# Kernel optimization log

Hardware: AMD Instinct MI355X
Metric: run time of the kernel (lower is better)

Reference implementation:

```python
import jax, jax.numpy as jnp
import numpy as np
from functools import partial

P = 14          # patch size
IMG = 448       # image size
D = 1152        # hidden dim
H = 16          # num heads
DH = D // H     # head dim = 72
I = 4304        # intermediate dim
L = 4           # num layers
N = (IMG // P) ** 2  # 1024 patches
EPS = 1e-6


def setup_inputs() -> dict:
    key = jax.random.key(0)
    ks = jax.random.split(key, 24)
    s = 0.02
    inp = {
        "images": jax.random.normal(ks[0], (2, 2, IMG, IMG, 3), jnp.float32),
        "conv_w": jax.random.normal(ks[1], (P, P, 3, D), jnp.float32) * s,
        "conv_b": jnp.zeros((D,), jnp.float32),
        "pos_emb": jax.random.normal(ks[2], (N, D), jnp.float32) * s,
        # per-layer stacked parameters, leading axis L
        "ln1_g": jnp.ones((L, D), jnp.float32),
        "ln1_b": jnp.zeros((L, D), jnp.float32),
        "Wq": jax.random.normal(ks[3], (L, D, D), jnp.float32) * s,
        "bq": jnp.zeros((L, D), jnp.float32),
        "Wk": jax.random.normal(ks[4], (L, D, D), jnp.float32) * s,
        "bk": jnp.zeros((L, D), jnp.float32),
        "Wv": jax.random.normal(ks[5], (L, D, D), jnp.float32) * s,
        "bv": jnp.zeros((L, D), jnp.float32),
        "Wo": jax.random.normal(ks[6], (L, D, D), jnp.float32) * s,
        "bo": jnp.zeros((L, D), jnp.float32),
        "ln2_g": jnp.ones((L, D), jnp.float32),
        "ln2_b": jnp.zeros((L, D), jnp.float32),
        "W1": jax.random.normal(ks[7], (L, D, I), jnp.float32) * s,
        "b1": jnp.zeros((L, I), jnp.float32),
        "W2": jax.random.normal(ks[8], (L, I, D), jnp.float32) * s,
        "b2": jnp.zeros((L, D), jnp.float32),
        "lnf_g": jnp.ones((D,), jnp.float32),
        "lnf_b": jnp.zeros((D,), jnp.float32),
    }
    return inp


def _layernorm(x, g, b):
    mu = jnp.mean(x, axis=-1, keepdims=True)
    var = jnp.var(x, axis=-1, keepdims=True)
    return (x - mu) * jax.lax.rsqrt(var + EPS) * g + b


def _encoder(images, conv_w, conv_b, pos_emb, ln1_g, ln1_b, Wq, bq, Wk, bk,
             Wv, bv, Wo, bo, ln2_g, ln2_b, W1, b1, W2, b2, lnf_g, lnf_b):
    B, T = images.shape[0], images.shape[1]
    x = images.reshape((B * T,) + images.shape[2:])  # [BT, IMG, IMG, 3]
    # patch embedding: Conv2D stride=kernel=patch, VALID
    x = jax.lax.conv_general_dilated(
        x, conv_w, window_strides=(P, P), padding='VALID',
        dimension_numbers=('NHWC', 'HWIO', 'NHWC')) + conv_b
    x = x.reshape(B * T, N, D) + pos_emb  # add position embedding

    scale = 1.0 / jnp.sqrt(jnp.asarray(DH, x.dtype))

    def block(x, p):
        (g1, b1_, wq, bq_, wk, bk_, wv, bv_, wo, bo_, g2, b2_,
         w1, bm1, w2, bm2) = p
        h = _layernorm(x, g1, b1_)
        q = (h @ wq + bq_).reshape(-1, N, H, DH).transpose(0, 2, 1, 3)
        k = (h @ wk + bk_).reshape(-1, N, H, DH).transpose(0, 2, 1, 3)
        v = (h @ wv + bv_).reshape(-1, N, H, DH).transpose(0, 2, 1, 3)
        scores = jnp.einsum('bhqd,bhkd->bhqk', q, k) * scale
        probs = jax.nn.softmax(scores, axis=-1)
        attn = jnp.einsum('bhqk,bhkd->bhqd', probs, v)
        attn = attn.transpose(0, 2, 1, 3).reshape(-1, N, D)
        x = x + (attn @ wo + bo_)
        h = _layernorm(x, g2, b2_)
        h = jax.nn.gelu(h @ w1 + bm1, approximate=True) @ w2 + bm2
        return x + h, None

    params = (ln1_g, ln1_b, Wq, bq, Wk, bk, Wv, bv, Wo, bo,
              ln2_g, ln2_b, W1, b1, W2, b2)
    x, _ = jax.lax.scan(block, x, params)
    x = _layernorm(x, lnf_g, lnf_b)
    return x.reshape(B, T, N, D)


def reference(images, conv_w, conv_b, pos_emb, ln1_g, ln1_b, Wq, bq, Wk, bk,
              Wv, bv, Wo, bo, ln2_g, ln2_b, W1, b1, W2, b2, lnf_g, lnf_b):
    return _encoder(images, conv_w, conv_b, pos_emb, ln1_g, ln1_b, Wq, bq,
                    Wk, bk, Wv, bv, Wo, bo, ln2_g, ln2_b, W1, b1, W2, b2,
                    lnf_g, lnf_b)
```

## Files before the change

### kernel.cpp

```cpp
#include <hip/hip_runtime.h>
#include <hip/hip_bf16.h>
#include <stdint.h>
#include <math.h>

typedef __hip_bfloat16 bf16;
typedef __attribute__((ext_vector_type(4))) float floatx4;
typedef __attribute__((ext_vector_type(8))) __bf16 bf16x8;

typedef __attribute__((address_space(1))) void gvoid_t;
typedef __attribute__((address_space(3))) void lvoid_t;

__device__ __forceinline__ void gl_lds16(const void* g, void* l){
  __builtin_amdgcn_global_load_lds((gvoid_t*)g, (lvoid_t*)l, 16, 0, 0);
}

__device__ __forceinline__ float gelu_f(float v){
  float u = 0.7978845608028654f*(v + 0.044715f*v*v*v);
  float e = __expf(2.0f*u);
  return v*(1.0f - 1.0f/(e+1.0f));
}

template<int MODE>
__global__ __launch_bounds__(256,4)
void gemm_bf16(const bf16* __restrict__ A, const bf16* __restrict__ BT,
               const float* __restrict__ bias, void* __restrict__ C,
               int N, int K, int kc, float qs)
{
  __shared__ bf16 As[2][128*32];
  __shared__ bf16 Bs[2][128*32];
  const int tid  = threadIdx.x;
  const int wave = tid>>6, lane = tid&63;
  const int quad = lane>>4, l16 = lane&15;

  int bm, bn;
  {
    const int nx = gridDim.x;
    const int nwg = nx * gridDim.y;
    int lid = blockIdx.x + nx*blockIdx.y;
    const int q = nwg >> 3, r = nwg & 7;
    const int xcd = lid & 7, off = lid >> 3;
    lid = (xcd < r ? xcd*(q+1) : r*(q+1) + (xcd - r)*q) + off;
    const int per = nx << 3;
    const int g   = lid / per;
    const int rem = lid - g*per;
    bm = (g<<3) + (rem & 7);
    bn = rem >> 3;
  }
  const int m0 = bm*128, n0 = bn*128;

  const int s  = blockIdx.z;
  const int kb = s*kc;
  const int ke = min(K, kb + kc);
  const int wm = (wave&1)*64, wn = (wave>>1)*64;
  floatx4 acc[4][4] = {};
  const bf16* ag = A  + (size_t)(m0 + wave*32 + (lane>>2))*K + (lane&3)*8;
  const bf16* bg = BT + (size_t)(n0 + wave*32 + (lane>>2))*K + (lane&3)*8;
  const size_t row16 = (size_t)16*K;
  const int woff = wave*1024;

  gl_lds16(ag + kb,          As[0] + woff);
  gl_lds16(ag + kb + row16,  As[0] + woff + 512);
  gl_lds16(bg + kb,          Bs[0] + woff);
  gl_lds16(bg + kb + row16,  Bs[0] + woff + 512);

  int cur = 0;
  for (int k0=kb; k0<ke; k0+=32){
    __syncthreads();
    const int kn = k0 + 32;
    if (kn < ke){
      bf16* asn = As[cur^1] + woff;
      bf16* bsn = Bs[cur^1] + woff;
      gl_lds16(ag + kn,          asn);
      gl_lds16(ag + kn + row16,  asn + 512);
      gl_lds16(bg + kn,          bsn);
      gl_lds16(bg + kn + row16,  bsn + 512);
    }
    bf16x8 af[4], bfr[4];
#pragma unroll
    for (int i=0;i<4;i++) af[i]  = *(const bf16x8*)(As[cur] + (wm + i*16 + l16)*32 + quad*8);
#pragma unroll
    for (int j=0;j<4;j++) bfr[j] = *(const bf16x8*)(Bs[cur] + (wn + j*16 + l16)*32 + quad*8);
#pragma unroll
    for (int i=0;i<4;i++)
#pragma unroll
      for (int j=0;j<4;j++)
        acc[i][j] = __builtin_amdgcn_mfma_f32_16x16x32_bf16(af[i], bfr[j], acc[i][j], 0,0,0);
    cur ^= 1;
  }
  const float scale = (MODE==3 && n0<1152) ? qs : 1.0f;
#pragma unroll
  for (int i=0;i<4;i++){
    const int gr0 = m0 + wm + i*16 + quad*4;
#pragma unroll
    for (int j=0;j<4;j++){
      const int gc = n0 + wn + j*16 + l16;
      const float bv = (MODE!=4 || s==0) ? bias[gc] : 0.f;
#pragma unroll
      for (int r=0;r<4;r++){
        const int gr = gr0 + r;
        float v = acc[i][j][r] + bv;
        if constexpr (MODE==1) v = gelu_f(v);
        if constexpr (MODE==3) v *= scale;
        if constexpr (MODE==4){
          ((bf16*)C)[((size_t)s*4096 + gr)*N + gc] = __float2bfloat16(v);
        } else {
          ((bf16*)C)[(size_t)gr*N + gc] = __float2bfloat16(v);
        }
      }
    }
  }
}

template<int OUTF32, int WRITEX>
__global__ __launch_bounds__(256)
void ln_red(const float* __restrict__ base, unsigned bmask,
            const bf16* __restrict__ part, int ks,
            const float* __restrict__ g, const float* __restrict__ b,
            float* __restrict__ xw, void* __restrict__ out)
{
  const int row  = blockIdx.x*4 + (threadIdx.x>>6);
  const int lane = threadIdx.x & 63;
  const float2* br = (const float2*)base + (size_t)(row & bmask)*576;
  float2 v[9];
#pragma unroll
  for (int r=0;r<9;r++) v[r] = br[r*64+lane];
  for (int s=0;s<ks;s++){
    const __hip_bfloat162* pr = (const __hip_bfloat162*)part + ((size_t)s*4096 + row)*576;
#pragma unroll
    for (int r=0;r<9;r++){
      const float2 pv = __bfloat1622float2(pr[r*64+lane]);
      v[r].x += pv.x; v[r].y += pv.y;
    }
  }
  float sm=0.f, ss=0.f;
#pragma unroll
  for (int r=0;r<9;r++){
    sm += v[r].x + v[r].y;
    ss += v[r].x*v[r].x + v[r].y*v[r].y;
  }
#pragma unroll
  for (int m=1;m<64;m<<=1){ sm += __shfl_xor(sm,m,64); ss += __shfl_xor(ss,m,64); }
  const float mean = sm*(1.0f/1152.0f);
  const float rs = rsqrtf(ss*(1.0f/1152.0f) - mean*mean + 1e-6f);
  const float2* gr2 = (const float2*)g;
  const float2* br2 = (const float2*)b;
#pragma unroll
  for (int r=0;r<9;r++){
    const int c = r*64+lane;
    if constexpr (WRITEX) ((float2*)xw)[(size_t)row*576 + c] = v[r];
    const float2 gg = gr2[c], bb = br2[c];
    const float o0 = (v[r].x-mean)*rs*gg.x + bb.x;
    const float o1 = (v[r].y-mean)*rs*gg.y + bb.y;
    if constexpr (OUTF32){
      ((float2*)out)[(size_t)row*576 + c] = make_float2(o0, o1);
    } else {
      __hip_bfloat162 hv;
      hv.x = __float2bfloat16(o0); hv.y = __float2bfloat16(o1);
      ((__hip_bfloat162*)out)[(size_t)row*576 + c] = hv;
    }
  }
}

__global__ __launch_bounds__(256)
void im2col_kernel(const float* __restrict__ img, bf16* __restrict__ out)
{
  const int idx = blockIdx.x*256 + threadIdx.x;
  const int kk = idx % 608;
  const int rr = idx / 608;
  float v = 0.f;
  if (kk < 588){
    const int bt = rr >> 10, n = rr & 1023;
    const int py = n >> 5, px = n & 31;
    const int ph = kk / 42;
    const int rem = kk - ph*42;
    const int pw = rem / 3;
    const int c  = rem - pw*3;
    v = img[(((size_t)bt*448 + py*14 + ph)*448 + px*14 + pw)*3 + c];
  }
  out[idx] = __float2bfloat16(v);
}

__global__ __launch_bounds__(256)
void transpose_cvt(const float* __restrict__ in, bf16* __restrict__ out,
                   int K, int N, int Kp, int Np)
{
  __shared__ float tile[32][33];
  const int nt = blockIdx.x*32, kt = blockIdx.y*32;
  const int r = threadIdx.x>>5, c = threadIdx.x&31;
#pragma unroll
  for (int i=0;i<4;i++){
    const int k = kt + r + i*8, n = nt + c;
    tile[r+i*8][c] = (k<K && n<N) ? in[(size_t)k*N + n] : 0.f;
  }
  __syncthreads();
#pragma unroll
  for (int i=0;i<4;i++){
    const int n = nt + r + i*8, k = kt + c;
    out[(size_t)n*Kp + k] = __float2bfloat16(tile[c][r+i*8]);
  }
}

__global__ __launch_bounds__(256)
void pack_biases(const float* __restrict__ bq, const float* __restrict__ bk,
                 const float* __restrict__ bv, const float* __restrict__ b1,
                 int l, float* __restrict__ bqkv, float* __restrict__ b1p,
                 float4* __restrict__ zbuf)
{
  const int i = blockIdx.x*256 + threadIdx.x;
  if (i < 3456){
    float v;
    if (i < 1152)      v = bq[l*1152 + i];
    else if (i < 2304) v = bk[l*1152 + i - 1152];
    else               v = bv[l*1152 + i - 2304];
    bqkv[i] = v;
  }
  if (i < 4352) b1p[i] = (i < 4304) ? b1[l*4304 + i] : 0.f;
  if (i == 0) *zbuf = make_float4(0.f,0.f,0.f,0.f);
}

__global__ __launch_bounds__(256)
void transpose_v(const bf16* __restrict__ src, bf16* __restrict__ dst)
{
  __shared__ bf16 tile[128][73];
  const int nc = blockIdx.x, bh = blockIdx.y;
  const int bt = bh>>4, hh = bh&15;
  const bf16* s = src + ((size_t)bt*1024 + nc*128)*3456 + 2304 + hh*72;
  for (int e=threadIdx.x; e<128*72; e+=256){
    const int n = e/72, dh = e - n*72;
    tile[n][dh] = s[(size_t)n*3456 + dh];
  }
  __syncthreads();
  bf16* d = dst + (size_t)bh*80*1024 + nc*128;
  const bf16 z = __float2bfloat16(0.f);
  for (int e=threadIdx.x; e<80*128; e+=256){
    const int dh = e>>7, n = e&127;
    d[(size_t)dh*1024 + n] = (dh<72) ? tile[n][dh] : z;
  }
}

__global__ __launch_bounds__(256,2)
void attn_kernel(const bf16* __restrict__ qkv, const bf16* __restrict__ vb,
                 const float4* __restrict__ zbuf, bf16* __restrict__ outp)
{
  __shared__ bf16 Ks[128*96];
  __shared__ bf16 Vs[80*128];
  __shared__ bf16 Ps[64*128];
  const int tid = threadIdx.x, wave = tid>>6, lane = tid&63;
  const int quad = lane>>4, l16 = lane&15;
  int lid = blockIdx.x + (blockIdx.y<<4);
  lid = ((lid & 7) << 7) + (lid >> 3);
  const int bh = lid >> 4, q0 = (lid & 15) << 6;
  const int bt = bh>>4, hh = bh&15;
  const bf16* vg = vb + (size_t)bh*80*1024;
  bf16x8 af0{}, af1{}, af2{};
  {
    const bf16* qp = qkv + (size_t)(bt*1024 + q0 + wave*16 + l16)*3456 + hh*72 + quad*8;
    af0 = *(const bf16x8*)(qp);
    af1 = *(const bf16x8*)(qp+32);
    if (quad==0) af2 = *(const bf16x8*)(qp+64);
  }
  float mr[4], lr[4];
#pragma unroll
  for (int r=0;r<4;r++){ mr[r] = -3.0e38f; lr[r] = 0.f; }
  floatx4 oacc[5] = {};
  for (int kc=0;kc<8;kc++){
    __syncthreads();
    {
      const char* kcb = (const char*)(qkv + (size_t)(bt*1024 + kc*128)*3456 + 1152 + hh*72);
#pragma unroll
      for (int i=0;i<6;i++){
        const int u = (wave*6+i)*64 + lane;
        const int row = u/12;
        const int pp = u - row*12;
        const int c = (pp & 12) | ((pp & 3) ^ (row & 3));
        const void* src = (c<9) ? (const void*)(kcb + (size_t)row*6912 + c*16)
                                : (const void*)zbuf;
        gl_lds16(src, (char*)Ks + (size_t)(wave*6+i)*1024);
      }
#pragma unroll
      for (int i=0;i<5;i++){
        const int u = (wave*5+i)*64 + lane;
        const int row = u>>4;
        const int pp = u & 15;
        const int c = (pp & 8) | ((pp & 7) ^ (row & 7));
        gl_lds16((const char*)vg + (size_t)row*2048 + kc*256 + c*16,
                 (char*)Vs + (size_t)(wave*5+i)*1024);
      }
    }
    __syncthreads();
    floatx4 sc[8] = {};
    const int ksw = (quad ^ (l16&3))*8;
#pragma unroll
    for (int ct=0;ct<8;ct++){
      const bf16* kr = Ks + (ct*16+l16)*96 + ksw;
      sc[ct] = __builtin_amdgcn_mfma_f32_16x16x32_bf16(af0, *(const bf16x8*)(kr   ), sc[ct],0,0,0);
      sc[ct] = __builtin_amdgcn_mfma_f32_16x16x32_bf16(af1, *(const bf16x8*)(kr+32), sc[ct],0,0,0);
      sc[ct] = __builtin_amdgcn_mfma_f32_16x16x32_bf16(af2, *(const bf16x8*)(kr+64), sc[ct],0,0,0);
    }
    float cm[4];
#pragma unroll
    for (int r=0;r<4;r++){
      cm[r] = sc[0][r];
#pragma unroll
      for (int ct=1;ct<8;ct++) cm[r] = fmaxf(cm[r], sc[ct][r]);
    }
#pragma unroll
    for (int off=1; off<16; off<<=1)
#pragma unroll
      for (int r=0;r<4;r++) cm[r] = fmaxf(cm[r], __shfl_xor(cm[r], off, 64));
    float al[4], ls[4];
#pragma unroll
    for (int r=0;r<4;r++){
      const float mn = fmaxf(mr[r], cm[r]);
      al[r] = exp2f(mr[r]-mn);
      mr[r] = mn; ls[r] = 0.f;
    }
#pragma unroll
    for (int ct=0;ct<8;ct++){
#pragma unroll
      for (int r=0;r<4;r++){
        const float pv = exp2f(sc[ct][r]-mr[r]);
        ls[r] += pv;
        const int row = wave*16+quad*4+r;
        const int c = ct*2 + (l16>>3);
        const int pp = (c & 8) | ((c & 7) ^ (row & 7));
        Ps[row*128 + pp*8 + (l16&7)] = __float2bfloat16(pv);
      }
    }
#pragma unroll
    for (int off=1; off<16; off<<=1)
#pragma unroll
      for (int r=0;r<4;r++) ls[r] += __shfl_xor(ls[r], off, 64);
#pragma unroll
    for (int r=0;r<4;r++) lr[r] = lr[r]*al[r] + ls[r];
#pragma unroll
    for (int t=0;t<5;t++)
#pragma unroll
      for (int r=0;r<4;r++) oacc[t][r] *= al[r];
    __syncthreads();
#pragma unroll
    for (int ks=0;ks<4;ks++){
      const int c = ks*4 + quad;
      const int pp = (c & 8) | ((c & 7) ^ (l16 & 7));
      const bf16x8 pf = *(const bf16x8*)(Ps + (wave*16+l16)*128 + pp*8);
#pragma unroll
      for (int t=0;t<5;t++){
        const bf16x8 vf = *(const bf16x8*)(Vs + (t*16+l16)*128 + pp*8);
        oacc[t] = __builtin_amdgcn_mfma_f32_16x16x32_bf16(pf, vf, oacc[t],0,0,0);
      }
    }
  }
#pragma unroll
  for (int t=0;t<5;t++){
    const int dh = t*16+l16;
    if (dh < 72){
#pragma unroll
      for (int r=0;r<4;r++){
        const int q = wave*16 + quad*4 + r;
        const float v = oacc[t][r] / lr[r];
        outp[((size_t)bt*1024 + q0 + q)*1152 + hh*72 + dh] = __float2bfloat16(v);
      }
    }
  }
}

extern "C" void kernel_launch(void* const* d_in, const int* in_sizes, int n_in,
                              void* d_out, int out_size, void* d_ws, size_t ws_size,
                              hipStream_t stream)
{
  (void)in_sizes; (void)n_in; (void)out_size; (void)ws_size;
  const float* images = (const float*)d_in[0];
  const float* conv_w = (const float*)d_in[1];
  const float* conv_b = (const float*)d_in[2];
  const float* pos_emb= (const float*)d_in[3];
  const float* ln1_g  = (const float*)d_in[4];
  const float* ln1_b  = (const float*)d_in[5];
  const float* Wq     = (const float*)d_in[6];
  const float* bq     = (const float*)d_in[7];
  const float* Wk     = (const float*)d_in[8];
  const float* bk     = (const float*)d_in[9];
  const float* Wv     = (const float*)d_in[10];
  const float* bv     = (const float*)d_in[11];
  const float* Wo     = (const float*)d_in[12];
  const float* bo     = (const float*)d_in[13];
  const float* ln2_g  = (const float*)d_in[14];
  const float* ln2_b  = (const float*)d_in[15];
  const float* W1     = (const float*)d_in[16];
  const float* b1     = (const float*)d_in[17];
  const float* W2     = (const float*)d_in[18];
  const float* b2     = (const float*)d_in[19];
  const float* lnf_g  = (const float*)d_in[20];
  const float* lnf_b  = (const float*)d_in[21];

  char* p = (char*)d_ws;
  auto take = [&](size_t nbytes)->char*{ char* q = p; p += (nbytes + 255) & ~(size_t)255; return q; };
  float* xw   = (float*)take(4096ull*1152*4);
  bf16* hbuf  = (bf16*) take(4096ull*1152*2);
  bf16* h1    = (bf16*) take(4096ull*4352*2);
  bf16* qkvr  = h1;
  bf16* vbuf  = (bf16*) take(64ull*80*1024*2);
  bf16* imcol = vbuf;
  bf16* aout  = (bf16*) take(4096ull*1152*2);
  bf16* WqkvT = (bf16*) take(3456ull*1152*2);
  bf16* WoT   = (bf16*) take(1152ull*1152*2);
  bf16* W1T   = (bf16*) take(4352ull*1152*2);
  bf16* cwT   = W1T;
  bf16* W2T   = (bf16*) take(1152ull*4352*2);
  bf16* Ppart = (bf16*) take(4ull*4096*1152*2);
  float* bqkv = (float*)take(3456*4);
  float* b1p  = (float*)take(4352*4);
  float4* zbuf= (float4*)take(256);

  const float qscale = 1.4426950408889634f / sqrtf(72.0f);

  im2col_kernel<<<9728, 256, 0, stream>>>(images, imcol);
  transpose_cvt<<<dim3(36,19), 256, 0, stream>>>(conv_w, cwT, 588, 1152, 608, 1152);
  gemm_bf16<4><<<dim3(9,32,2), 256, 0, stream>>>(imcol, cwT, conv_b, Ppart, 1152, 608, 320, 0.f);

  for (int l=0;l<4;l++){
    transpose_cvt<<<dim3(36,36), 256, 0, stream>>>(Wq + (size_t)l*1152*1152, WqkvT,                1152,1152,1152,1152);
    transpose_cvt<<<dim3(36,36), 256, 0, stream>>>(Wk + (size_t)l*1152*1152, WqkvT + 1152ull*1152, 1152,1152,1152,1152);
    transpose_cvt<<<dim3(36,36), 256, 0, stream>>>(Wv + (size_t)l*1152*1152, WqkvT + 2304ull*1152, 1152,1152,1152,1152);
    transpose_cvt<<<dim3(36,36), 256, 0, stream>>>(Wo + (size_t)l*1152*1152, WoT, 1152,1152,1152,1152);
    transpose_cvt<<<dim3(136,36),256, 0, stream>>>(W1 + (size_t)l*1152*4304, W1T, 1152,4304,1152,4352);
    transpose_cvt<<<dim3(36,136),256, 0, stream>>>(W2 + (size_t)l*4304*1152, W2T, 4304,1152,4352,1152);
    pack_biases<<<17,256,0,stream>>>(bq,bk,bv,b1,l,bqkv,b1p,zbuf);

    if (l==0)
      ln_red<0,1><<<1024,256,0,stream>>>(pos_emb, 1023u, Ppart, 2, ln1_g, ln1_b, xw, hbuf);
    else
      ln_red<0,1><<<1024,256,0,stream>>>(xw, 4095u, Ppart, 4, ln1_g + l*1152, ln1_b + l*1152, xw, hbuf);

    gemm_bf16<3><<<dim3(27,32,1),256,0,stream>>>(hbuf, WqkvT, bqkv, qkvr, 3456, 1152, 1152, qscale);
    transpose_v<<<dim3(8,64),256,0,stream>>>(qkvr, vbuf);
    attn_kernel<<<dim3(16,64),256,0,stream>>>(qkvr, vbuf, zbuf, aout);
    gemm_bf16<4><<<dim3(9,32,3),256,0,stream>>>(aout, WoT, bo + l*1152, Ppart, 1152, 1152, 384, 0.f);
    ln_red<0,1><<<1024,256,0,stream>>>(xw, 4095u, Ppart, 3, ln2_g + l*1152, ln2_b + l*1152, xw, hbuf);

    gemm_bf16<1><<<dim3(34,32,1),256,0,stream>>>(hbuf, W1T, b1p, h1, 4352, 1152, 1152, 0.f);
    gemm_bf16<4><<<dim3(9,32,4),256,0,stream>>>(h1, W2T, b2 + l*1152, Ppart, 1152, 4352, 1088, 0.f);
  }
  ln_red<1,0><<<1024,256,0,stream>>>(xw, 4095u, Ppart, 4, lnf_g, lnf_b, nullptr, (float*)d_out);
}
```

Before: 1.625 ms.

## Deepen GEMM LDS pipeline to four stages with XOR swizzle and single barrier

Replaces the double-buffered GEMM main loop with a four-buffer ring in a 64KB LDS array. Three stages are prefetched ahead, gated by an explicit vmcnt wait plus one barrier per step, and the LDS layout gets an XOR swizzle to avoid bank conflicts on fragment reads. MFMA blocks are wrapped in raised wave priority, and launch bounds drop to 2 workgroups per CU to fit the larger LDS footprint. This trades occupancy for deeper latency hiding. The tail re-issues loads of the last tile rather than branching.

```diff
diff --git a/kernel.cpp b/kernel.cpp
--- a/kernel.cpp
+++ b/kernel.cpp
@@ -21,13 +21,12 @@
 }
 
 template<int MODE>
-__global__ __launch_bounds__(256,4)
+__global__ __launch_bounds__(256,2)
 void gemm_bf16(const bf16* __restrict__ A, const bf16* __restrict__ BT,
                const float* __restrict__ bias, void* __restrict__ C,
                int N, int K, int kc, float qs)
 {
-  __shared__ bf16 As[2][128*32];
-  __shared__ bf16 Bs[2][128*32];
+  __shared__ __align__(128) char ldsm[65536];
   const int tid  = threadIdx.x;
   const int wave = tid>>6, lane = tid&63;
   const int quad = lane>>4, l16 = lane&15;
@@ -51,42 +50,53 @@
   const int s  = blockIdx.z;
   const int kb = s*kc;
   const int ke = min(K, kb + kc);
+  const int T  = (ke - kb) >> 5;
   const int wm = (wave&1)*64, wn = (wave>>1)*64;
   floatx4 acc[4][4] = {};
-  const bf16* ag = A  + (size_t)(m0 + wave*32 + (lane>>2))*K + (lane&3)*8;
-  const bf16* bg = BT + (size_t)(n0 + wave*32 + (lane>>2))*K + (lane&3)*8;
-  const size_t row16 = (size_t)16*K;
-  const int woff = wave*1024;
-
-  gl_lds16(ag + kb,          As[0] + woff);
-  gl_lds16(ag + kb + row16,  As[0] + woff + 512);
-  gl_lds16(bg + kb,          Bs[0] + woff);
-  gl_lds16(bg + kb + row16,  Bs[0] + woff + 512);
-
-  int cur = 0;
-  for (int k0=kb; k0<ke; k0+=32){
-    __syncthreads();
-    const int kn = k0 + 32;
-    if (kn < ke){
-      bf16* asn = As[cur^1] + woff;
-      bf16* bsn = Bs[cur^1] + woff;
-      gl_lds16(ag + kn,          asn);
-      gl_lds16(ag + kn + row16,  asn + 512);
-      gl_lds16(bg + kn,          bsn);
-      gl_lds16(bg + kn + row16,  bsn + 512);
-    }
+
+  const int grow  = tid>>2;
+  const int gslot = (tid&3) ^ (grow&3);
+  const bf16* aBase = A  + (size_t)(m0 + grow)*K + kb + gslot*8;
+  const bf16* bBase = BT + (size_t)(n0 + grow)*K + kb + gslot*8;
+  const size_t rowK64 = (size_t)64*K;
+  char* ldw = ldsm + (wave<<10);
+
+  const int swz = (quad ^ (l16&3))<<4;
+  const int aRd = ((wm + l16)<<6) + swz;
+  const int bRd = ((wn + l16)<<6) + swz + 8192;
+
+  auto stage = [&](int tp){
+    char* ld = ldw + ((tp&3)<<14);
+    const bf16* ga = aBase + (size_t)tp*32;
+    const bf16* gb = bBase + (size_t)tp*32;
+    gl_lds16(ga,          ld);
+    gl_lds16(ga + rowK64, ld + 4096);
+    gl_lds16(gb,          ld + 8192);
+    gl_lds16(gb + rowK64, ld + 12288);
+  };
+
+  stage(0); stage(1); stage(2);
+
+  for (int t=0; t<T; ++t){
+    asm volatile("s_waitcnt vmcnt(8)" ::: "memory");
+    asm volatile("s_barrier" ::: "memory");
+    const char* bufb = ldsm + ((t&3)<<14);
     bf16x8 af[4], bfr[4];
 #pragma unroll
-    for (int i=0;i<4;i++) af[i]  = *(const bf16x8*)(As[cur] + (wm + i*16 + l16)*32 + quad*8);
-#pragma unroll
-    for (int j=0;j<4;j++) bfr[j] = *(const bf16x8*)(Bs[cur] + (wn + j*16 + l16)*32 + quad*8);
+    for (int i=0;i<4;i++) af[i]  = *(const bf16x8*)(bufb + aRd + (i<<10));
+#pragma unroll
+    for (int j=0;j<4;j++) bfr[j] = *(const bf16x8*)(bufb + bRd + (j<<10));
+    stage(min(t+3, T-1));
+    __builtin_amdgcn_s_setprio(1);
 #pragma unroll
     for (int i=0;i<4;i++)
 #pragma unroll
       for (int j=0;j<4;j++)
         acc[i][j] = __builtin_amdgcn_mfma_f32_16x16x32_bf16(af[i], bfr[j], acc[i][j], 0,0,0);
-    cur ^= 1;
-  }
+    __builtin_amdgcn_s_setprio(0);
+  }
+  asm volatile("s_waitcnt vmcnt(0)" ::: "memory");
+
   const float scale = (MODE==3 && n0<1152) ? qs : 1.0f;
 #pragma unroll
   for (int i=0;i<4;i++){
```

Measured after the change: 1.636 ms. About the same (+0.7%).
